# Performance work log

Hardware: AMD Instinct MI355X
Metric: run time of the kernel (lower is better)

Reference implementation:

```python
import jax, jax.numpy as jnp
import numpy as np
from jax import lax

B, S, D = 4, 2048, 256      # batch, seq_len, hidden_dim
F = 1024                    # ffn_dim
E = 32                      # num_experts
K = 4                       # top_k


def setup_inputs() -> dict:
    key = jax.random.key(0)
    ks = jax.random.split(key, 5)
    scale = 0.02
    x = jax.random.normal(ks[0], (B, S, D), dtype=jnp.float32)
    router_w = jax.random.normal(ks[1], (E, D), dtype=jnp.float32) * scale   # gate Linear weight [out=E, in=D]
    w_gate = jax.random.normal(ks[2], (E, F, D), dtype=jnp.float32) * scale  # per-expert [F, D]
    w_up = jax.random.normal(ks[3], (E, F, D), dtype=jnp.float32) * scale
    w_down = jax.random.normal(ks[4], (E, D, F), dtype=jnp.float32) * scale
    return {"x": x, "router_w": router_w, "w_gate": w_gate, "w_up": w_up, "w_down": w_down}


def reference(x, router_w, w_gate, w_up, w_down):
    # Eval mode: jitter noise and dropout are inactive (training-only in the source).
    b, s, d = x.shape
    T = b * s
    xf = x.reshape(T, d)                                   # [T, D]

    # --- Router ---
    logits = xf @ router_w.T                               # [T, E]
    tk_logits, tk_idx = lax.top_k(logits, K)               # [T, K]
    tk_w = jax.nn.softmax(tk_logits, axis=-1)              # [T, K]
    probs = jax.nn.softmax(logits, axis=-1)                # [T, E]
    one_hot = jax.nn.one_hot(tk_idx, E, dtype=x.dtype)     # [T, K, E]
    tokens_per_expert = one_hot.sum(axis=(0, 1))           # [E]
    f_frac = tokens_per_expert / T
    P = probs.mean(axis=0)
    aux_loss = E * (f_frac * P).sum()

    # combine[t, e] = sum_k tk_w[t,k] * [tk_idx[t,k] == e]
    combine = jnp.einsum("tk,tke->te", tk_w, one_hot)      # [T, E]

    # --- Experts: scan over experts, SwiGLU FFN, weighted accumulate ---
    def step(acc, params):
        wg, wu, wd, ce = params                            # [F,D], [F,D], [D,F], [T]
        h = jax.nn.silu(xf @ wg.T) * (xf @ wu.T)           # [T, F]
        return acc + ce[:, None] * (h @ wd.T), None

    out, _ = lax.scan(step, jnp.zeros_like(xf),
                      (w_gate, w_up, w_down, combine.T))
    return out.reshape(b, s, d), aux_loss
```

## Files before the change

### kernel.cpp

```cpp
#include <hip/hip_runtime.h>
#include <math.h>

#define TOK 8192
#define DIM 256
#define NE  32
#define NK  4
#define NF  1024

typedef __bf16 bf16x8 __attribute__((ext_vector_type(8)));
typedef float  f32x4  __attribute__((ext_vector_type(4)));
typedef unsigned short u16x8 __attribute__((ext_vector_type(8)));

__device__ __forceinline__ unsigned short f2b(float f) {
  unsigned u = __builtin_bit_cast(unsigned, f);
  unsigned r = (u + 0x7FFFu + ((u >> 16) & 1u)) >> 16;
  return (unsigned short)r;
}

__device__ __forceinline__ void gload16(const void* g, void* l) {
  __builtin_amdgcn_global_load_lds(
      (const __attribute__((address_space(1))) void*)g,
      (__attribute__((address_space(3))) void*)l, 16, 0, 0);
}

__global__ __launch_bounds__(256) void router_kernel(
    const float* __restrict__ x, const float* __restrict__ rw,
    int* __restrict__ counts, float* __restrict__ psum,
    int* __restrict__ etok, float* __restrict__ ewt,
    float* __restrict__ outz)
{
  __shared__ float xs[32][DIM + 4];
  __shared__ float ws[NE][DIM + 4];
  __shared__ float lg[32][NE];
  __shared__ int hist[NE];
  __shared__ int base[NE];

  const int tid = threadIdx.x;
  const int t0 = blockIdx.x * 32;

  {
    float4 z4 = {0.f, 0.f, 0.f, 0.f};
    float4* og = (float4*)(outz + (size_t)t0 * DIM);
    #pragma unroll
    for (int i = 0; i < 8; i++) og[i*256 + tid] = z4;
  }

  {
    const float4* xg = (const float4*)(x + (size_t)t0 * DIM);
    for (int i = tid; i < 32 * (DIM/4); i += 256) {
      int t = i / (DIM/4), c = i % (DIM/4);
      *(float4*)&xs[t][c*4] = xg[t*(DIM/4)+c];
    }
    const float4* wgp = (const float4*)rw;
    for (int i = tid; i < NE * (DIM/4); i += 256) {
      int e = i / (DIM/4), c = i % (DIM/4);
      *(float4*)&ws[e][c*4] = wgp[e*(DIM/4)+c];
    }
  }
  if (tid < NE) hist[tid] = 0;
  __syncthreads();

  for (int i = 0; i < 4; i++) {
    int idx = i*256 + tid;
    int t = idx >> 5, e = idx & 31;
    float acc = 0.f;
    for (int c = 0; c < DIM/4; c++) {
      float4 a = *(const float4*)&xs[t][c*4];
      float4 b = *(const float4*)&ws[e][c*4];
      acc += a.x*b.x + a.y*b.y + a.z*b.z + a.w*b.w;
    }
    lg[t][e] = acc;
  }
  __syncthreads();

  int ids[NK]; int slots[NK]; float wts[NK];
  if (tid < 32) {
    const int t = tid;
    float l[NE];
    #pragma unroll
    for (int e = 0; e < NE; e++) l[e] = lg[t][e];
    unsigned mask = 0;
    float vals[NK];
    #pragma unroll
    for (int k = 0; k < NK; k++) {
      float best = -INFINITY; int bi = 0;
      for (int e = 0; e < NE; e++)
        if (!((mask >> e) & 1u) && l[e] > best) { best = l[e]; bi = e; }
      mask |= 1u << bi; vals[k] = best; ids[k] = bi;
    }
    float s4 = 0.f;
    #pragma unroll
    for (int k = 0; k < NK; k++) { wts[k] = __expf(vals[k] - vals[0]); s4 += wts[k]; }
    #pragma unroll
    for (int k = 0; k < NK; k++) wts[k] /= s4;
    float s = 0.f;
    for (int e = 0; e < NE; e++) { l[e] = __expf(l[e] - vals[0]); s += l[e]; }
    float inv = 1.f / s;
    for (int e = 0; e < NE; e++) lg[t][e] = l[e] * inv;
    #pragma unroll
    for (int k = 0; k < NK; k++) slots[k] = atomicAdd(&hist[ids[k]], 1);
  }
  __syncthreads();
  if (tid < NE) {
    float s = 0.f;
    for (int t = 0; t < 32; t++) s += lg[t][tid];
    atomicAdd(&psum[tid], s);
    int h = hist[tid];
    base[tid] = h ? atomicAdd(&counts[tid], h) : 0;
  }
  __syncthreads();
  if (tid < 32) {
    #pragma unroll
    for (int k = 0; k < NK; k++) {
      int p = base[ids[k]] + slots[k];
      etok[(size_t)ids[k]*TOK + p] = t0 + tid;
      ewt [(size_t)ids[k]*TOK + p] = wts[k];
    }
  }
}

__global__ void aux_kernel(const int* __restrict__ counts,
                           const float* __restrict__ psum,
                           float* __restrict__ aux_out)
{
  int tid = threadIdx.x;
  float v = 0.f;
  if (tid < NE) v = (counts[tid] / (float)TOK) * (psum[tid] / (float)TOK);
  #pragma unroll
  for (int off = 32; off; off >>= 1) v += __shfl_down(v, off);
  if (tid == 0) aux_out[0] = (float)NE * v;
}

__global__ __launch_bounds__(256) void convert_kernel(
    const float* __restrict__ wg_, const float* __restrict__ wu_,
    const float* __restrict__ wd_, unsigned short* __restrict__ wB)
{
  int gid = blockIdx.x * 256 + threadIdx.x;
  int sg  = gid >> 11;
  int idx = gid & 2047;
  int e   = sg / 48;
  int st  = sg - e * 48;
  int ch  = st / 3;
  int ty  = st - ch * 3;
  unsigned short* dst = wB + ((size_t)sg << 14);
  const float* src;
  int pos;
  if (ty < 2) {
    int f = idx >> 5, gk = idx & 31;
    const float* w = (ty == 0) ? wg_ : wu_;
    src = w + (size_t)e * (NF*DIM) + (size_t)(ch*64 + f) * DIM + (gk << 3);
    pos = f*256 + ((gk ^ (f & 7)) << 3);
  } else {
    int d = idx >> 3, fg = idx & 7;
    src = wd_ + (size_t)e * (DIM*NF) + (size_t)d * NF + (ch << 6) + (fg << 3);
    pos = (d << 6) + ((fg ^ (d & 7)) << 3);
  }
  float4 a = *(const float4*)src;
  float4 c = *(const float4*)(src + 4);
  u16x8 v;
  v[0]=f2b(a.x); v[1]=f2b(a.y); v[2]=f2b(a.z); v[3]=f2b(a.w);
  v[4]=f2b(c.x); v[5]=f2b(c.y); v[6]=f2b(c.z); v[7]=f2b(c.w);
  *(u16x8*)&dst[pos] = v;
}

#define PWB(N) asm volatile("s_waitcnt vmcnt(" #N ") lgkmcnt(0)\n\ts_barrier" ::: "memory")

#define ISSUE(s_) do {                                                  \
    const unsigned short* sp_ = wE + ((size_t)(s_) << 14);              \
    unsigned short* dp_ = &ring[(s_) & 3][0];                           \
    _Pragma("unroll")                                                   \
    for (int i_ = 0; i_ < 4; i_++) {                                    \
      int o_ = (i_*512 + tid) << 3;                                     \
      gload16(sp_ + o_, dp_ + o_);                                      \
    }                                                                   \
  } while (0)

#define COMP_G(rs)                                                      \
  _Pragma("unroll")                                                     \
  for (int nt = 0; nt < 2; nt++) {                                      \
    const int fl = nw*32 + nt*16 + ln;                                  \
    const int rowb = fl*256, xo = fl & 7;                               \
    ga[nt][0] = (f32x4){0,0,0,0}; ga[nt][1] = (f32x4){0,0,0,0};         \
    _Pragma("unroll")                                                   \
    for (int kk = 0; kk < 8; kk++) {                                    \
      bf16x8 bg = *(const bf16x8*)&rs[rowb + (((kk*4 + q) ^ xo) << 3)]; \
      ga[nt][0] = __builtin_amdgcn_mfma_f32_16x16x32_bf16(xf[0][kk], bg, ga[nt][0], 0,0,0); \
      ga[nt][1] = __builtin_amdgcn_mfma_f32_16x16x32_bf16(xf[1][kk], bg, ga[nt][1], 0,0,0); \
    }                                                                   \
  }

#define COMP_U(rs)                                                      \
  _Pragma("unroll")                                                     \
  for (int nt = 0; nt < 2; nt++) {                                      \
    const int fl = nw*32 + nt*16 + ln;                                  \
    const int rowb = fl*256, xo = fl & 7;                               \
    f32x4 ua0 = (f32x4){0,0,0,0}, ua1 = (f32x4){0,0,0,0};               \
    _Pragma("unroll")                                                   \
    for (int kk = 0; kk < 8; kk++) {                                    \
      bf16x8 bu = *(const bf16x8*)&rs[rowb + (((kk*4 + q) ^ xo) << 3)]; \
      ua0 = __builtin_amdgcn_mfma_f32_16x16x32_bf16(xf[0][kk], bu, ua0, 0,0,0); \
      ua1 = __builtin_amdgcn_mfma_f32_16x16x32_bf16(xf[1][kk], bu, ua1, 0,0,0); \
    }                                                                   \
    _Pragma("unroll")                                                   \
    for (int rr = 0; rr < 4; rr++) {                                    \
      float g0 = ga[nt][0][rr], g1 = ga[nt][1][rr];                     \
      hs[mw*32      + q*4 + rr][fl] = f2b((g0 / (1.f + __expf(-g0))) * ua0[rr]); \
      hs[mw*32 + 16 + q*4 + rr][fl] = f2b((g1 / (1.f + __expf(-g1))) * ua1[rr]); \
    }                                                                   \
  }

#define COMP_D(rs)                                                      \
  _Pragma("unroll")                                                     \
  for (int kk = 0; kk < 2; kk++) {                                      \
    bf16x8 a0 = *(const bf16x8*)&hs[mw*32      + ln][kk*32 + q*8];      \
    bf16x8 a1 = *(const bf16x8*)&hs[mw*32 + 16 + ln][kk*32 + q*8];      \
    _Pragma("unroll")                                                   \
    for (int nt = 0; nt < 8; nt++) {                                    \
      const int d = nw*128 + nt*16 + ln;                                \
      bf16x8 bd = *(const bf16x8*)&rs[d*64 + (((kk*4 + q) ^ (d & 7)) << 3)]; \
      oacc[nt][0] = __builtin_amdgcn_mfma_f32_16x16x32_bf16(a0, bd, oacc[nt][0], 0,0,0); \
      oacc[nt][1] = __builtin_amdgcn_mfma_f32_16x16x32_bf16(a1, bd, oacc[nt][1], 0,0,0); \
    }                                                                   \
  }

__global__ __launch_bounds__(512, 2) void expert_mfma6_kernel(
    const float* __restrict__ x,
    const unsigned short* __restrict__ wB,
    const int* __restrict__ counts,
    const int* __restrict__ etok, const float* __restrict__ ewt,
    float* __restrict__ out)
{
  const int b  = blockIdx.x;
  const int j  = b >> 3;
  const int e  = (b & 7) + 8 * (j & 3);
  const int s0 = j >> 2;
  const int cnt = counts[e];

  __shared__ unsigned short ring[4][16384];
  __shared__ unsigned short hs[128][72];
  __shared__ int   lel[128];
  __shared__ float lwt[128];

  const int tid  = threadIdx.x;
  const int lane = tid & 63;
  const int wv   = tid >> 6;
  const int mw   = wv & 3;
  const int nw   = wv >> 2;
  const int q    = lane >> 4;
  const int ln   = lane & 15;

  const unsigned short* wE = wB + (size_t)e * 48 * 16384;
  const int*   el = etok + (size_t)e * TOK;
  const float* ew = ewt  + (size_t)e * TOK;

  for (int t0 = s0 * 128; t0 < cnt; t0 += 1024) {
    if (tid < 128) {
      int gt = t0 + tid;
      lel[tid] = (gt < cnt) ? el[gt] : -1;
      lwt[tid] = (gt < cnt) ? ew[gt] : 0.f;
    }
    __syncthreads();

    bf16x8 xf[2][8];
    #pragma unroll
    for (int m = 0; m < 2; m++) {
      int row = mw*32 + m*16 + ln;
      int tok = lel[row]; if (tok < 0) tok = 0;
      const float* xr = x + (size_t)tok * DIM;
      #pragma unroll
      for (int k = 0; k < 8; k++) {
        float4 a = *(const float4*)(xr + k*32 + q*8);
        float4 c = *(const float4*)(xr + k*32 + q*8 + 4);
        union { bf16x8 v; unsigned short s[8]; } t;
        t.s[0]=f2b(a.x); t.s[1]=f2b(a.y); t.s[2]=f2b(a.z); t.s[3]=f2b(a.w);
        t.s[4]=f2b(c.x); t.s[5]=f2b(c.y); t.s[6]=f2b(c.z); t.s[7]=f2b(c.w);
        xf[m][k] = t.v;
      }
    }

    f32x4 oacc[8][2];
    #pragma unroll
    for (int nt = 0; nt < 8; nt++) { oacc[nt][0] = (f32x4){0,0,0,0}; oacc[nt][1] = (f32x4){0,0,0,0}; }

    ISSUE(0); ISSUE(1); ISSUE(2);

    f32x4 ga[2][2];

    #pragma unroll 1
    for (int ch = 0; ch < 15; ch++) {
      const int sb = 3*ch;
      PWB(8); ISSUE(sb+3);
      { const unsigned short* rs = ring[(sb  ) & 3]; COMP_G(rs); }
      PWB(8); ISSUE(sb+4);
      { const unsigned short* rs = ring[(sb+1) & 3]; COMP_U(rs); }
      PWB(8); ISSUE(sb+5);
      { const unsigned short* rs = ring[(sb+2) & 3]; COMP_D(rs); }
    }
    PWB(8); { const unsigned short* rs = ring[1]; COMP_G(rs); }
    PWB(4); { const unsigned short* rs = ring[2]; COMP_U(rs); }
    PWB(0); { const unsigned short* rs = ring[3]; COMP_D(rs); }

    #pragma unroll
    for (int nt = 0; nt < 8; nt++) {
      int d = nw*128 + nt*16 + ln;
      #pragma unroll
      for (int m = 0; m < 2; m++)
        #pragma unroll
        for (int rr = 0; rr < 4; rr++) {
          int tl = mw*32 + m*16 + q*4 + rr;
          int tok = lel[tl];
          if (tok >= 0)
            atomicAdd(&out[(size_t)tok*DIM + d], lwt[tl] * oacc[nt][m][rr]);
        }
    }
    __syncthreads();
  }
}

__global__ __launch_bounds__(512, 2) void expert_mfma5_kernel(
    const float* __restrict__ x,
    const float* __restrict__ wg_, const float* __restrict__ wu_,
    const float* __restrict__ wd_,
    const int* __restrict__ counts,
    const int* __restrict__ etok, const float* __restrict__ ewt,
    float* __restrict__ out)
{
  const int b  = blockIdx.x;
  const int j  = b >> 3;
  const int e  = (b & 7) + 8 * (j & 3);
  const int s0 = j >> 2;
  const int cnt = counts[e];

  __shared__ unsigned short stg[2][16384];
  __shared__ unsigned short hs[128][72];
  __shared__ int   lel[128];
  __shared__ float lwt[128];

  const int tid  = threadIdx.x;
  const int lane = tid & 63;
  const int wv   = tid >> 6;
  const int mw   = wv & 3;
  const int nw   = wv >> 2;
  const int q    = lane >> 4;
  const int ln   = lane & 15;

  int guOff[4], dOff[4], dRow[4], dFg[4];
  #pragma unroll
  for (int i = 0; i < 4; i++) {
    int G = i*512 + tid;
    int f = G >> 5, gk = G & 31;
    guOff[i] = f*256 + ((gk ^ (f & 7)) << 3);
    int d = G >> 3, fg = G & 7;
    dOff[i] = d*64 + ((fg ^ (d & 7)) << 3);
    dRow[i] = d; dFg[i] = fg;
  }

  const float* wgE = wg_ + (size_t)e * NF * DIM;
  const float* wuE = wu_ + (size_t)e * NF * DIM;
  const float* wdE = wd_ + (size_t)e * DIM * NF;

  const int*   el = etok + (size_t)e * TOK;
  const float* ew = ewt  + (size_t)e * TOK;

  for (int t0 = s0 * 128; t0 < cnt; t0 += 1024) {
    if (tid < 128) {
      int gt = t0 + tid;
      lel[tid] = (gt < cnt) ? el[gt] : -1;
      lwt[tid] = (gt < cnt) ? ew[gt] : 0.f;
    }
    __syncthreads();

    bf16x8 xf[2][8];
    #pragma unroll
    for (int m = 0; m < 2; m++) {
      int row = mw*32 + m*16 + ln;
      int tok = lel[row]; if (tok < 0) tok = 0;
      const float* xr = x + (size_t)tok * DIM;
      #pragma unroll
      for (int k = 0; k < 8; k++) {
        float4 a = *(const float4*)(xr + k*32 + q*8);
        float4 c = *(const float4*)(xr + k*32 + q*8 + 4);
        union { bf16x8 v; unsigned short s[8]; } t;
        t.s[0]=f2b(a.x); t.s[1]=f2b(a.y); t.s[2]=f2b(a.z); t.s[3]=f2b(a.w);
        t.s[4]=f2b(c.x); t.s[5]=f2b(c.y); t.s[6]=f2b(c.z); t.s[7]=f2b(c.w);
        xf[m][k] = t.v;
      }
    }

    f32x4 oacc[8][2];
    #pragma unroll
    for (int nt = 0; nt < 8; nt++) { oacc[nt][0] = (f32x4){0,0,0,0}; oacc[nt][1] = (f32x4){0,0,0,0}; }

    unsigned short* pA = stg[0];
    unsigned short* pB = stg[1];
    float4 r[8];

    {
      const float4* s4 = (const float4*)wgE;
      #pragma unroll
      for (int i = 0; i < 4; i++) { int G = i*512 + tid; r[2*i] = s4[2*G]; r[2*i+1] = s4[2*G+1]; }
      #pragma unroll
      for (int i = 0; i < 4; i++) {
        u16x8 v;
        v[0]=f2b(r[2*i].x);   v[1]=f2b(r[2*i].y);   v[2]=f2b(r[2*i].z);   v[3]=f2b(r[2*i].w);
        v[4]=f2b(r[2*i+1].x); v[5]=f2b(r[2*i+1].y); v[6]=f2b(r[2*i+1].z); v[7]=f2b(r[2*i+1].w);
        *(u16x8*)&pA[guOff[i]] = v;
      }
    }
    __syncthreads();

    f32x4 ga[2][2];

    for (int ch = 0; ch < 16; ch++) {
      {
        const float4* s4 = (const float4*)(wuE + (size_t)ch*16384);
        #pragma unroll
        for (int i = 0; i < 4; i++) { int G = i*512 + tid; r[2*i] = s4[2*G]; r[2*i+1] = s4[2*G+1]; }
      }
      #pragma unroll
      for (int nt = 0; nt < 2; nt++) {
        int fl = nw*32 + nt*16 + ln;
        int rowb = fl*256, xo = fl & 7;
        ga[nt][0] = (f32x4){0,0,0,0}; ga[nt][1] = (f32x4){0,0,0,0};
        #pragma unroll
        for (int kk = 0; kk < 8; kk++) {
          bf16x8 bg = *(const bf16x8*)&pA[rowb + (((kk*4 + q) ^ xo) << 3)];
          ga[nt][0] = __builtin_amdgcn_mfma_f32_16x16x32_bf16(xf[0][kk], bg, ga[nt][0], 0,0,0);
          ga[nt][1] = __builtin_amdgcn_mfma_f32_16x16x32_bf16(xf[1][kk], bg, ga[nt][1], 0,0,0);
        }
      }
      #pragma unroll
      for (int i = 0; i < 4; i++) {
        u16x8 v;
        v[0]=f2b(r[2*i].x);   v[1]=f2b(r[2*i].y);   v[2]=f2b(r[2*i].z);   v[3]=f2b(r[2*i].w);
        v[4]=f2b(r[2*i+1].x); v[5]=f2b(r[2*i+1].y); v[6]=f2b(r[2*i+1].z); v[7]=f2b(r[2*i+1].w);
        *(u16x8*)&pB[guOff[i]] = v;
      }
      __syncthreads();
      { unsigned short* t = pA; pA = pB; pB = t; }

      {
        #pragma unroll
        for (int i = 0; i < 4; i++) {
          const float4* p = (const float4*)(wdE + (size_t)dRow[i]*NF + ch*64 + dFg[i]*8);
          r[2*i] = p[0]; r[2*i+1] = p[1];
        }
      }
      #pragma unroll
      for (int nt = 0; nt < 2; nt++) {
        int fl = nw*32 + nt*16 + ln;
        int rowb = fl*256, xo = fl & 7;
        f32x4 ua0 = (f32x4){0,0,0,0}, ua1 = (f32x4){0,0,0,0};
        #pragma unroll
        for (int kk = 0; kk < 8; kk++) {
          bf16x8 bu = *(const bf16x8*)&pA[rowb + (((kk*4 + q) ^ xo) << 3)];
          ua0 = __builtin_amdgcn_mfma_f32_16x16x32_bf16(xf[0][kk], bu, ua0, 0,0,0);
          ua1 = __builtin_amdgcn_mfma_f32_16x16x32_bf16(xf[1][kk], bu, ua1, 0,0,0);
        }
        #pragma unroll
        for (int rr = 0; rr < 4; rr++) {
          float g0 = ga[nt][0][rr], g1 = ga[nt][1][rr];
          hs[mw*32      + q*4 + rr][fl] = f2b((g0 / (1.f + __expf(-g0))) * ua0[rr]);
          hs[mw*32 + 16 + q*4 + rr][fl] = f2b((g1 / (1.f + __expf(-g1))) * ua1[rr]);
        }
      }
      #pragma unroll
      for (int i = 0; i < 4; i++) {
        u16x8 v;
        v[0]=f2b(r[2*i].x);   v[1]=f2b(r[2*i].y);   v[2]=f2b(r[2*i].z);   v[3]=f2b(r[2*i].w);
        v[4]=f2b(r[2*i+1].x); v[5]=f2b(r[2*i+1].y); v[6]=f2b(r[2*i+1].z); v[7]=f2b(r[2*i+1].w);
        *(u16x8*)&pB[dOff[i]] = v;
      }
      __syncthreads();
      { unsigned short* t = pA; pA = pB; pB = t; }

      if (ch < 15) {
        const float4* s4 = (const float4*)(wgE + (size_t)(ch+1)*16384);
        #pragma unroll
        for (int i = 0; i < 4; i++) { int G = i*512 + tid; r[2*i] = s4[2*G]; r[2*i+1] = s4[2*G+1]; }
      }
      #pragma unroll
      for (int kk = 0; kk < 2; kk++) {
        bf16x8 a0 = *(const bf16x8*)&hs[mw*32      + ln][kk*32 + q*8];
        bf16x8 a1 = *(const bf16x8*)&hs[mw*32 + 16 + ln][kk*32 + q*8];
        #pragma unroll
        for (int nt = 0; nt < 8; nt++) {
          int d = nw*128 + nt*16 + ln;
          bf16x8 bd = *(const bf16x8*)&pA[d*64 + (((kk*4 + q) ^ (d & 7)) << 3)];
          oacc[nt][0] = __builtin_amdgcn_mfma_f32_16x16x32_bf16(a0, bd, oacc[nt][0], 0,0,0);
          oacc[nt][1] = __builtin_amdgcn_mfma_f32_16x16x32_bf16(a1, bd, oacc[nt][1], 0,0,0);
        }
      }
      if (ch < 15) {
        #pragma unroll
        for (int i = 0; i < 4; i++) {
          u16x8 v;
          v[0]=f2b(r[2*i].x);   v[1]=f2b(r[2*i].y);   v[2]=f2b(r[2*i].z);   v[3]=f2b(r[2*i].w);
          v[4]=f2b(r[2*i+1].x); v[5]=f2b(r[2*i+1].y); v[6]=f2b(r[2*i+1].z); v[7]=f2b(r[2*i+1].w);
          *(u16x8*)&pB[guOff[i]] = v;
        }
      }
      __syncthreads();
      { unsigned short* t = pA; pA = pB; pB = t; }
    }

    #pragma unroll
    for (int nt = 0; nt < 8; nt++) {
      int d = nw*128 + nt*16 + ln;
      #pragma unroll
      for (int m = 0; m < 2; m++)
        #pragma unroll
        for (int rr = 0; rr < 4; rr++) {
          int tl = mw*32 + m*16 + q*4 + rr;
          int tok = lel[tl];
          if (tok >= 0)
            atomicAdd(&out[(size_t)tok*DIM + d], lwt[tl] * oacc[nt][m][rr]);
        }
    }
    __syncthreads();
  }
}

extern "C" void kernel_launch(void* const* d_in, const int* in_sizes, int n_in,
                              void* d_out, int out_size, void* d_ws, size_t ws_size,
                              hipStream_t stream)
{
  const float* x  = (const float*)d_in[0];
  const float* rw = (const float*)d_in[1];
  const float* wg = (const float*)d_in[2];
  const float* wu = (const float*)d_in[3];
  const float* wd = (const float*)d_in[4];
  float* out = (float*)d_out;

  int*   counts = (int*)d_ws;
  float* psum   = (float*)((char*)d_ws + 128);
  int*   etok   = (int*)((char*)d_ws + 256);
  float* ewt    = (float*)((char*)d_ws + 256 + (size_t)NE*TOK*4);

  hipMemsetAsync(d_ws, 0, 256, stream);

  router_kernel<<<TOK/32, 256, 0, stream>>>(x, rw, counts, psum, etok, ewt, out);
  aux_kernel<<<1, 64, 0, stream>>>(counts, psum, out + (size_t)TOK*DIM);

  const size_t wboff = (size_t)4 << 20;
  const size_t wbsz  = (size_t)NE * 48 * 16384 * 2;
  if (ws_size >= wboff + wbsz) {
    unsigned short* wB = (unsigned short*)((char*)d_ws + wboff);
    convert_kernel<<<(NE*48*2048)/256, 256, 0, stream>>>(wg, wu, wd, wB);
    expert_mfma6_kernel<<<256, 512, 0, stream>>>(x, wB, counts, etok, ewt, out);
  } else {
    expert_mfma5_kernel<<<256, 512, 0, stream>>>(x, wg, wu, wd, counts, etok, ewt, out);
  }
}
```

Before: 367.6 us.

## Balance expert work across blocks by splitting tiles along FFN chunks

Replaces the fixed mapping of each block to one expert and a strided set of 128-token tiles with a global work list. Each (expert, token tile, FFN chunk) unit is one of 16 chunks per tile, and the flattened list is divided evenly across the 256 blocks, so blocks with imbalanced expert counts no longer straggle. A block may handle a partial range of FFN chunks for a tile and accumulate its partial down-projection through atomics. This adds a serial prefix computation, a per-unit expert search, and repeated loading of x and token lists for partial tiles.

```diff
diff --git a/kernel.cpp b/kernel.cpp
--- a/kernel.cpp
+++ b/kernel.cpp
@@ -165,15 +165,21 @@
 
 #define PWB(N) asm volatile("s_waitcnt vmcnt(" #N ") lgkmcnt(0)\n\ts_barrier" ::: "memory")
 
-#define ISSUE(s_) do {                                                  \
-    const unsigned short* sp_ = wE + ((size_t)(s_) << 14);              \
-    unsigned short* dp_ = &ring[(s_) & 3][0];                           \
+#define ISSUE_L(sl_) do {                                               \
+    const unsigned short* sp_ = wE + ((size_t)(3*c0 + (sl_)) << 14);    \
+    unsigned short* dp_ = &ring[(sl_) & 3][0];                          \
     _Pragma("unroll")                                                   \
     for (int i_ = 0; i_ < 4; i_++) {                                    \
       int o_ = (i_*512 + tid) << 3;                                     \
       gload16(sp_ + o_, dp_ + o_);                                      \
     }                                                                   \
   } while (0)
+
+#define WI(sl_) do { const int ah_ = S - (sl_);                         \
+    if (ah_ > 3)       { PWB(8); ISSUE_L((sl_) + 3); }                  \
+    else if (ah_ == 3) { PWB(8); }                                      \
+    else if (ah_ == 2) { PWB(4); }                                      \
+    else               { PWB(0); } } while (0)
 
 #define COMP_G(rs)                                                      \
   _Pragma("unroll")                                                     \
@@ -223,23 +229,18 @@
     }                                                                   \
   }
 
-__global__ __launch_bounds__(512, 2) void expert_mfma6_kernel(
+__global__ __launch_bounds__(512, 2) void expert_mfma7_kernel(
     const float* __restrict__ x,
     const unsigned short* __restrict__ wB,
     const int* __restrict__ counts,
     const int* __restrict__ etok, const float* __restrict__ ewt,
     float* __restrict__ out)
 {
-  const int b  = blockIdx.x;
-  const int j  = b >> 3;
-  const int e  = (b & 7) + 8 * (j & 3);
-  const int s0 = j >> 2;
-  const int cnt = counts[e];
-
   __shared__ unsigned short ring[4][16384];
   __shared__ unsigned short hs[128][72];
   __shared__ int   lel[128];
   __shared__ float lwt[128];
+  __shared__ int   pfx[NE + 1];
 
   const int tid  = threadIdx.x;
   const int lane = tid & 63;
@@ -249,11 +250,35 @@
   const int q    = lane >> 4;
   const int ln   = lane & 15;
 
-  const unsigned short* wE = wB + (size_t)e * 48 * 16384;
-  const int*   el = etok + (size_t)e * TOK;
-  const float* ew = ewt  + (size_t)e * TOK;
-
-  for (int t0 = s0 * 128; t0 < cnt; t0 += 1024) {
+  if (tid == 0) {
+    int acc = 0;
+    #pragma unroll 1
+    for (int e = 0; e < NE; e++) { pfx[e] = acc; acc += (counts[e] + 127) >> 7; }
+    pfx[NE] = acc;
+  }
+  __syncthreads();
+
+  const int U  = __builtin_amdgcn_readfirstlane(pfx[NE] << 4);
+  const int ub = ((blockIdx.x & 7) << 5) | (blockIdx.x >> 3);
+  int       u  = (ub * U) >> 8;
+  const int u1 = ((ub + 1) * U) >> 8;
+
+  #pragma unroll 1
+  while (u < u1) {
+    const int g = u >> 4;
+    int ev = 0;
+    #pragma unroll 1
+    while (pfx[ev + 1] <= g) ev++;
+    const int e   = __builtin_amdgcn_readfirstlane(ev);
+    const int t   = __builtin_amdgcn_readfirstlane(g - pfx[e]);
+    const int c0  = u & 15;
+    const int c1  = (16 < c0 + (u1 - u)) ? 16 : (c0 + (u1 - u));
+    const int cnt = __builtin_amdgcn_readfirstlane(counts[e]);
+    const int t0  = t << 7;
+    const unsigned short* wE = wB + (size_t)e * 48 * 16384;
+    const int*   el = etok + (size_t)e * TOK;
+    const float* ew = ewt  + (size_t)e * TOK;
+
     if (tid < 128) {
       int gt = t0 + tid;
       lel[tid] = (gt < cnt) ? el[gt] : -1;
@@ -271,10 +296,10 @@
       for (int k = 0; k < 8; k++) {
         float4 a = *(const float4*)(xr + k*32 + q*8);
         float4 c = *(const float4*)(xr + k*32 + q*8 + 4);
-        union { bf16x8 v; unsigned short s[8]; } t;
-        t.s[0]=f2b(a.x); t.s[1]=f2b(a.y); t.s[2]=f2b(a.z); t.s[3]=f2b(a.w);
-        t.s[4]=f2b(c.x); t.s[5]=f2b(c.y); t.s[6]=f2b(c.z); t.s[7]=f2b(c.w);
-        xf[m][k] = t.v;
+        union { bf16x8 v; unsigned short s[8]; } tt;
+        tt.s[0]=f2b(a.x); tt.s[1]=f2b(a.y); tt.s[2]=f2b(a.z); tt.s[3]=f2b(a.w);
+        tt.s[4]=f2b(c.x); tt.s[5]=f2b(c.y); tt.s[6]=f2b(c.z); tt.s[7]=f2b(c.w);
+        xf[m][k] = tt.v;
       }
     }
 
@@ -282,23 +307,20 @@
     #pragma unroll
     for (int nt = 0; nt < 8; nt++) { oacc[nt][0] = (f32x4){0,0,0,0}; oacc[nt][1] = (f32x4){0,0,0,0}; }
 
-    ISSUE(0); ISSUE(1); ISSUE(2);
+    const int S = 3 * (c1 - c0);
+
+    asm volatile("s_waitcnt vmcnt(0)" ::: "memory");
+    ISSUE_L(0); ISSUE_L(1); ISSUE_L(2);
 
     f32x4 ga[2][2];
 
     #pragma unroll 1
-    for (int ch = 0; ch < 15; ch++) {
-      const int sb = 3*ch;
-      PWB(8); ISSUE(sb+3);
-      { const unsigned short* rs = ring[(sb  ) & 3]; COMP_G(rs); }
-      PWB(8); ISSUE(sb+4);
-      { const unsigned short* rs = ring[(sb+1) & 3]; COMP_U(rs); }
-      PWB(8); ISSUE(sb+5);
-      { const unsigned short* rs = ring[(sb+2) & 3]; COMP_D(rs); }
-    }
-    PWB(8); { const unsigned short* rs = ring[1]; COMP_G(rs); }
-    PWB(4); { const unsigned short* rs = ring[2]; COMP_U(rs); }
-    PWB(0); { const unsigned short* rs = ring[3]; COMP_D(rs); }
+    for (int c = c0; c < c1; c++) {
+      const int sb = 3 * (c - c0);
+      WI(sb    ); { const unsigned short* rs = ring[ sb      & 3]; COMP_G(rs); }
+      WI(sb + 1); { const unsigned short* rs = ring[(sb + 1) & 3]; COMP_U(rs); }
+      WI(sb + 2); { const unsigned short* rs = ring[(sb + 2) & 3]; COMP_D(rs); }
+    }
 
     #pragma unroll
     for (int nt = 0; nt < 8; nt++) {
@@ -314,6 +336,8 @@
         }
     }
     __syncthreads();
+
+    u += c1 - c0;
   }
 }
 
@@ -547,7 +571,7 @@
   if (ws_size >= wboff + wbsz) {
     unsigned short* wB = (unsigned short*)((char*)d_ws + wboff);
     convert_kernel<<<(NE*48*2048)/256, 256, 0, stream>>>(wg, wu, wd, wB);
-    expert_mfma6_kernel<<<256, 512, 0, stream>>>(x, wB, counts, etok, ewt, out);
+    expert_mfma7_kernel<<<256, 512, 0, stream>>>(x, wB, counts, etok, ewt, out);
   } else {
     expert_mfma5_kernel<<<256, 512, 0, stream>>>(x, wg, wu, wd, counts, etok, ewt, out);
   }
```

After: 317.5 us. 13.6% less time.
